# Kernel tuning notes

Measured on AMD Instinct MI355X. Metric: run time of the kernel, lower is better.

The kernel has to match this reference:

```python
import jax, jax.numpy as jnp
import numpy as np

N = 50000
E = 800000
IN_CH = 128
HID = 16
HEADS = 8
OUT_CH = 64
NEG_SLOPE = 0.2


def setup_inputs() -> dict:
    key = jax.random.key(0)
    ks = jax.random.split(key, 16)
    x = jax.random.normal(ks[0], (N, IN_CH), dtype=jnp.float32)
    edge_index = jax.random.randint(ks[1], (2, E), 0, N, dtype=jnp.int64)
    s = 0.05
    # GATv2 layer 1: in=128 -> heads=8, out=16 (concat -> 128)
    W1l = jax.random.normal(ks[2], (IN_CH, HEADS * HID), dtype=jnp.float32) * s
    b1l = jnp.zeros((HEADS * HID,), dtype=jnp.float32)
    W1r = jax.random.normal(ks[3], (IN_CH, HEADS * HID), dtype=jnp.float32) * s
    b1r = jnp.zeros((HEADS * HID,), dtype=jnp.float32)
    att1 = jax.random.normal(ks[4], (HEADS, HID), dtype=jnp.float32) * s
    bias1 = jnp.zeros((HEADS * HID,), dtype=jnp.float32)
    # GATv2 layer 2: in=128 -> heads=1, out=64
    W2l = jax.random.normal(ks[5], (HEADS * HID, OUT_CH), dtype=jnp.float32) * s
    b2l = jnp.zeros((OUT_CH,), dtype=jnp.float32)
    W2r = jax.random.normal(ks[6], (HEADS * HID, OUT_CH), dtype=jnp.float32) * s
    b2r = jnp.zeros((OUT_CH,), dtype=jnp.float32)
    att2 = jax.random.normal(ks[7], (1, OUT_CH), dtype=jnp.float32) * s
    bias2 = jnp.zeros((OUT_CH,), dtype=jnp.float32)
    return dict(x=x, edge_index=edge_index,
                W1l=W1l, b1l=b1l, W1r=W1r, b1r=b1r, att1=att1, bias1=bias1,
                W2l=W2l, b2l=b2l, W2r=W2r, b2r=b2r, att2=att2, bias2=bias2)


def gatv2_conv(x, src, dst, Wl, bl, Wr, br, att, bias, heads, out_ch, concat):
    n = x.shape[0]
    xl = (x @ Wl + bl).reshape(n, heads, out_ch)  # source transform
    xr = (x @ Wr + br).reshape(n, heads, out_ch)  # target transform
    m = xl[src] + xr[dst]                          # [E, H, C]
    m = jnp.where(m > 0, m, NEG_SLOPE * m)         # LeakyReLU(0.2)
    alpha = jnp.einsum('ehc,hc->eh', m, att)       # [E, H]
    # segment softmax over destination nodes (every node has a self loop)
    amax = jax.ops.segment_max(alpha, dst, num_segments=n)
    ea = jnp.exp(alpha - amax[dst])
    denom = jax.ops.segment_sum(ea, dst, num_segments=n)
    w = ea / denom[dst]                            # [E, H]
    out = jax.ops.segment_sum(xl[src] * w[:, :, None], dst, num_segments=n)
    if concat:
        out = out.reshape(n, heads * out_ch)
    else:
        out = out.mean(axis=1)
    return out + bias


def reference(x, edge_index, W1l, b1l, W1r, b1r, att1, bias1,
              W2l, b2l, W2r, b2r, att2, bias2):
    n = x.shape[0]
    loops = jnp.arange(n, dtype=edge_index.dtype)
    src = jnp.concatenate([edge_index[0], loops])
    dst = jnp.concatenate([edge_index[1], loops])
    # dropout layers are identity in eval mode
    h = gatv2_conv(x, src, dst, W1l, b1l, W1r, b1r, att1, bias1,
                   heads=HEADS, out_ch=HID, concat=True)
    h = jax.nn.elu(h)
    out = gatv2_conv(h, src, dst, W2l, b2l, W2r, b2r, att2, bias2,
                     heads=1, out_ch=OUT_CH, concat=True)
    return out
```

## Files before the change

kernel.cpp:

```cpp
#include <hip/hip_runtime.h>
#include <hip/hip_bf16.h>

constexpr int N_  = 50000;
constexpr int E_  = 800000;
constexpr int ET_ = 850000;
constexpr float NEG_SLOPE = 0.2f;

constexpr int SCAN_NB = (N_ + 255) / 256;
constexpr int CSR_CAP = 1250008;
constexpr int HT      = ET_ / 8;
constexpr int HB      = (HT + 255) / 256;
constexpr int G1B     = N_ / 16;
constexpr int ZERO4   = (50000 + CSR_CAP) / 4;

typedef __attribute__((ext_vector_type(8))) short short8;
typedef __attribute__((ext_vector_type(4))) float f32x4;

__device__ inline float leaky(float v) { return fmaxf(v, NEG_SLOPE * v); }

__device__ inline unsigned bf16rn(float f) {
    union { float f; unsigned u; } v; v.f = f;
    return (v.u + 0x7fffu + ((v.u >> 16) & 1u)) >> 16;
}
__device__ inline float2 unpack2(unsigned u) {
    return make_float2(__uint_as_float(u << 16), __uint_as_float(u & 0xffff0000u));
}

__device__ inline int edge_dst(int e, const int* __restrict__ ei) {
    return (e < E_) ? ei[E_ + e] : e - E_;
}
__device__ inline int edge_src(int e, const int* __restrict__ ei) {
    return (e < E_) ? ei[e] : e - E_;
}

__global__ __launch_bounds__(256) void init_kernel(
        const float* __restrict__ W1l, const float* __restrict__ W1r,
        const float* __restrict__ W2l, const float* __restrict__ W2r,
        unsigned short* __restrict__ wsw, unsigned short* __restrict__ wsw2,
        int4* __restrict__ zbase) {
    int gid = blockIdx.x * 256 + threadIdx.x;
    if (gid < ZERO4) zbase[gid] = make_int4(0, 0, 0, 0);
    if (gid < 32768) {
        int j    = gid & 7;
        int lane = (gid >> 3) & 63;
        int ks   = (gid >> 9) & 3;
        int ct   = gid >> 11;
        int k = ks * 32 + ((lane >> 4) & 3) * 8 + j;
        int c = ct * 16 + (lane & 15);
        float v = (c < 128) ? W1l[k * 128 + c] : W1r[k * 128 + (c - 128)];
        wsw[gid] = (unsigned short)bf16rn(v);
    } else if (gid < 49152) {
        int t2   = gid - 32768;
        int j    = t2 & 7;
        int lane = (t2 >> 3) & 63;
        int ks   = (t2 >> 9) & 3;
        int ct   = t2 >> 11;
        int k = ks * 32 + ((lane >> 4) & 3) * 8 + j;
        int c = ct * 16 + (lane & 15);
        float v = (c < 64) ? W2l[k * 64 + c] : W2r[k * 64 + (c - 64)];
        wsw2[t2] = (unsigned short)bf16rn(v);
    }
}

__global__ __launch_bounds__(256) void hist_gemm1(
        const int* __restrict__ ei, int* __restrict__ count, int* __restrict__ off,
        const float* __restrict__ x, const unsigned short* __restrict__ wsw,
        const float* __restrict__ bl, const float* __restrict__ br,
        unsigned short* __restrict__ xlu, float* __restrict__ xr1) {
    if (blockIdx.x < HB) {
        int t = blockIdx.x * 256 + threadIdx.x;
        if (t >= HT) return;
        int e8 = t * 8;
        int d[8], o[8];
        #pragma unroll
        for (int i = 0; i < 8; ++i) d[i] = edge_dst(e8 + i, ei);
        #pragma unroll
        for (int i = 0; i < 8; ++i) o[i] = atomicAdd(&count[d[i]], 1);
        int4* op = (int4*)(off + e8);
        op[0] = make_int4(o[0], o[1], o[2], o[3]);
        op[1] = make_int4(o[4], o[5], o[6], o[7]);
        return;
    }
    const int blk  = blockIdx.x - HB;
    const int wave = threadIdx.x >> 6;
    const int lane = threadIdx.x & 63;
    const int n0 = blk * 16;
    const int m = lane & 15;
    const int q = (lane >> 4) & 3;
    const float* __restrict__ arow = x + (size_t)(n0 + m) * 128 + q * 8;
    short8 afrag[4];
    #pragma unroll
    for (int ks = 0; ks < 4; ++ks) {
        float4 v0 = *(const float4*)(arow + ks * 32);
        float4 v1 = *(const float4*)(arow + ks * 32 + 4);
        short8 a;
        a[0] = (short)bf16rn(v0.x); a[1] = (short)bf16rn(v0.y);
        a[2] = (short)bf16rn(v0.z); a[3] = (short)bf16rn(v0.w);
        a[4] = (short)bf16rn(v1.x); a[5] = (short)bf16rn(v1.y);
        a[6] = (short)bf16rn(v1.z); a[7] = (short)bf16rn(v1.w);
        afrag[ks] = a;
    }
    #pragma unroll
    for (int i = 0; i < 4; ++i) {
        const int ct = wave * 4 + i;
        f32x4 acc = {0.f, 0.f, 0.f, 0.f};
        #pragma unroll
        for (int ks = 0; ks < 4; ++ks) {
            short8 b = *(const short8*)(wsw + ((size_t)(ct * 4 + ks) * 64 + lane) * 8);
            acc = __builtin_amdgcn_mfma_f32_16x16x32_bf16(afrag[ks], b, acc, 0, 0, 0);
        }
        const int col = ct * 16 + m;
        if (ct < 8) {
            float bias = bl[col];
            #pragma unroll
            for (int j = 0; j < 4; ++j) {
                int row = n0 + q * 4 + j;
                xlu[(size_t)row * 128 + col] = (unsigned short)bf16rn(acc[j] + bias);
            }
        } else {
            float bias = br[col - 128];
            #pragma unroll
            for (int j = 0; j < 4; ++j) {
                int row = n0 + q * 4 + j;
                xr1[(size_t)row * 128 + (col - 128)] = acc[j] + bias;
            }
        }
    }
}

__global__ __launch_bounds__(256) void scan_partial(
        const int* __restrict__ count, int* __restrict__ bsum) {
    __shared__ int red[256];
    int t = threadIdx.x;
    int i = blockIdx.x * 256 + t;
    red[t] = (i < N_) ? ((count[i] + 7) & ~7) : 0;
    __syncthreads();
    #pragma unroll
    for (int o = 128; o > 0; o >>= 1) {
        if (t < o) red[t] += red[t + o];
        __syncthreads();
    }
    if (t == 0) bsum[blockIdx.x] = red[0];
}

__global__ __launch_bounds__(256) void scan_final2(
        const int* __restrict__ count, const int* __restrict__ bsum,
        int* __restrict__ start) {
    __shared__ int top[256];
    __shared__ int buf[256];
    int t = threadIdx.x;
    top[t] = (t < SCAN_NB) ? bsum[t] : 0;
    __syncthreads();
    #pragma unroll
    for (int o = 1; o < 256; o <<= 1) {
        int add = (t >= o) ? top[t - o] : 0;
        __syncthreads();
        top[t] += add;
        __syncthreads();
    }
    int bst = (blockIdx.x == 0) ? 0 : top[blockIdx.x - 1];
    int i = blockIdx.x * 256 + t;
    int v = (i < N_) ? ((count[i] + 7) & ~7) : 0;
    buf[t] = v;
    __syncthreads();
    #pragma unroll
    for (int o = 1; o < 256; o <<= 1) {
        int add = (t >= o) ? buf[t - o] : 0;
        __syncthreads();
        buf[t] += add;
        __syncthreads();
    }
    if (i < N_) start[i] = bst + buf[t] - v;
}

__global__ __launch_bounds__(256) void scatter_kernel(
        const int* __restrict__ ei, const int* __restrict__ start,
        const int* __restrict__ off, int* __restrict__ csr_src) {
    int t = blockIdx.x * 256 + threadIdx.x;
    if (t >= HT) return;
    int e8 = t * 8;
    int4 o0 = *(const int4*)(off + e8);
    int4 o1 = *(const int4*)(off + e8 + 4);
    int o[8] = {o0.x, o0.y, o0.z, o0.w, o1.x, o1.y, o1.z, o1.w};
    int s[8], d[8];
    #pragma unroll
    for (int i = 0; i < 8; ++i) {
        s[i] = edge_src(e8 + i, ei);
        d[i] = edge_dst(e8 + i, ei);
    }
    int st[8];
    #pragma unroll
    for (int i = 0; i < 8; ++i) st[i] = start[d[i]];
    #pragma unroll
    for (int i = 0; i < 8; ++i) csr_src[st[i] + o[i]] = s[i];
}

__global__ __launch_bounds__(256) void fused1(
        const int* __restrict__ csr_src, const int* __restrict__ start,
        const int* __restrict__ count,
        const unsigned* __restrict__ xl1b, const float* __restrict__ xr1,
        const float* __restrict__ att, const float* __restrict__ bias1,
        float* __restrict__ hout) {
    int t = blockIdx.x * 256 + threadIdx.x;
    int n = __builtin_amdgcn_readfirstlane(t >> 6);
    int lane = t & 63;
    if (n >= N_) return;
    float2 xr = *(const float2*)(xr1 + (size_t)n * 128 + 2 * lane);
    float2 av = *(const float2*)(att + 2 * lane);
    int p0 = __builtin_amdgcn_readfirstlane(start[n]);
    int p1 = p0 + __builtin_amdgcn_readfirstlane(count[n]);
    float2 acc = make_float2(0.f, 0.f);
    float l = 0.f;
    for (int p = p0; p < p1; p += 4) {
        int4 si = *(const int4*)(csr_src + p);
        int s0 = __builtin_amdgcn_readfirstlane(si.x);
        int s1 = __builtin_amdgcn_readfirstlane(si.y);
        int s2 = __builtin_amdgcn_readfirstlane(si.z);
        int s3 = __builtin_amdgcn_readfirstlane(si.w);
        float2 x0 = unpack2(xl1b[(size_t)s0 * 64 + lane]);
        float2 x1 = unpack2(xl1b[(size_t)s1 * 64 + lane]);
        float2 x2 = unpack2(xl1b[(size_t)s2 * 64 + lane]);
        float2 x3 = unpack2(xl1b[(size_t)s3 * 64 + lane]);
        float a0 = fmaf(leaky(x0.x + xr.x), av.x, leaky(x0.y + xr.y) * av.y);
        float a1 = fmaf(leaky(x1.x + xr.x), av.x, leaky(x1.y + xr.y) * av.y);
        float a2 = fmaf(leaky(x2.x + xr.x), av.x, leaky(x2.y + xr.y) * av.y);
        float a3 = fmaf(leaky(x3.x + xr.x), av.x, leaky(x3.y + xr.y) * av.y);
        a0 += __shfl_xor(a0, 1); a1 += __shfl_xor(a1, 1);
        a2 += __shfl_xor(a2, 1); a3 += __shfl_xor(a3, 1);
        a0 += __shfl_xor(a0, 2); a1 += __shfl_xor(a1, 2);
        a2 += __shfl_xor(a2, 2); a3 += __shfl_xor(a3, 2);
        a0 += __shfl_xor(a0, 4); a1 += __shfl_xor(a1, 4);
        a2 += __shfl_xor(a2, 4); a3 += __shfl_xor(a3, 4);
        float w0 = __expf(a0);
        float w1 = p + 1 < p1 ? __expf(a1) : 0.f;
        float w2 = p + 2 < p1 ? __expf(a2) : 0.f;
        float w3 = p + 3 < p1 ? __expf(a3) : 0.f;
        acc.x = fmaf(w0, x0.x, acc.x); acc.y = fmaf(w0, x0.y, acc.y); l += w0;
        acc.x = fmaf(w1, x1.x, acc.x); acc.y = fmaf(w1, x1.y, acc.y); l += w1;
        acc.x = fmaf(w2, x2.x, acc.x); acc.y = fmaf(w2, x2.y, acc.y); l += w2;
        acc.x = fmaf(w3, x3.x, acc.x); acc.y = fmaf(w3, x3.y, acc.y); l += w3;
    }
    float2 bv = *(const float2*)(bias1 + 2 * lane);
    float vx = acc.x / l + bv.x;
    float vy = acc.y / l + bv.y;
    float2 o;
    o.x = vx > 0.f ? vx : (__expf(vx) - 1.f);
    o.y = vy > 0.f ? vy : (__expf(vy) - 1.f);
    *(float2*)(hout + (size_t)n * 128 + 2 * lane) = o;
}

__global__ __launch_bounds__(256) void gemm2_mfma(
        const float* __restrict__ hbuf,
        const unsigned short* __restrict__ wsw2,
        const float* __restrict__ bl, const float* __restrict__ br,
        unsigned short* __restrict__ xlu2, float* __restrict__ xr2) {
    const int wave = threadIdx.x >> 6;
    const int lane = threadIdx.x & 63;
    const int n0 = blockIdx.x * 16;
    const int m = lane & 15;
    const int q = (lane >> 4) & 3;
    const float* __restrict__ arow = hbuf + (size_t)(n0 + m) * 128 + q * 8;
    short8 afrag[4];
    #pragma unroll
    for (int ks = 0; ks < 4; ++ks) {
        float4 v0 = *(const float4*)(arow + ks * 32);
        float4 v1 = *(const float4*)(arow + ks * 32 + 4);
        short8 a;
        a[0] = (short)bf16rn(v0.x); a[1] = (short)bf16rn(v0.y);
        a[2] = (short)bf16rn(v0.z); a[3] = (short)bf16rn(v0.w);
        a[4] = (short)bf16rn(v1.x); a[5] = (short)bf16rn(v1.y);
        a[6] = (short)bf16rn(v1.z); a[7] = (short)bf16rn(v1.w);
        afrag[ks] = a;
    }
    #pragma unroll
    for (int i = 0; i < 2; ++i) {
        const int ct = wave * 2 + i;
        f32x4 acc = {0.f, 0.f, 0.f, 0.f};
        #pragma unroll
        for (int ks = 0; ks < 4; ++ks) {
            short8 b = *(const short8*)(wsw2 + ((size_t)(ct * 4 + ks) * 64 + lane) * 8);
            acc = __builtin_amdgcn_mfma_f32_16x16x32_bf16(afrag[ks], b, acc, 0, 0, 0);
        }
        const int col = ct * 16 + m;
        if (ct < 4) {
            float bias = bl[col];
            #pragma unroll
            for (int j = 0; j < 4; ++j) {
                int row = n0 + q * 4 + j;
                xlu2[(size_t)row * 64 + col] = (unsigned short)bf16rn(acc[j] + bias);
            }
        } else {
            float bias = br[col - 64];
            #pragma unroll
            for (int j = 0; j < 4; ++j) {
                int row = n0 + q * 4 + j;
                xr2[(size_t)row * 64 + (col - 64)] = acc[j] + bias;
            }
        }
    }
}

__global__ __launch_bounds__(256) void fused2(
        const int* __restrict__ csr_src, const int* __restrict__ start,
        const int* __restrict__ count,
        const unsigned* __restrict__ xl2b, const float* __restrict__ xr2,
        const float* __restrict__ att, const float* __restrict__ bias2,
        float* __restrict__ out) {
    int t = blockIdx.x * 256 + threadIdx.x;
    int n = __builtin_amdgcn_readfirstlane(t >> 6);
    int lane = t & 63;
    int half = lane >> 5;
    int lc   = lane & 31;
    if (n >= N_) return;
    float2 xr = *(const float2*)(xr2 + (size_t)n * 64 + 2 * lc);
    float2 av = *(const float2*)(att + 2 * lc);
    int p0 = __builtin_amdgcn_readfirstlane(start[n]);
    int p1 = p0 + __builtin_amdgcn_readfirstlane(count[n]);
    float2 acc = make_float2(0.f, 0.f);
    float l = 0.f;
    for (int p = p0; p < p1; p += 8) {
        int4 ia = *(const int4*)(csr_src + p);
        int4 ib = *(const int4*)(csr_src + p + 4);
        int sx[8];
        sx[0] = __builtin_amdgcn_readfirstlane(ia.x);
        sx[1] = __builtin_amdgcn_readfirstlane(ia.y);
        sx[2] = __builtin_amdgcn_readfirstlane(ia.z);
        sx[3] = __builtin_amdgcn_readfirstlane(ia.w);
        sx[4] = __builtin_amdgcn_readfirstlane(ib.x);
        sx[5] = __builtin_amdgcn_readfirstlane(ib.y);
        sx[6] = __builtin_amdgcn_readfirstlane(ib.z);
        sx[7] = __builtin_amdgcn_readfirstlane(ib.w);
        #pragma unroll
        for (int u = 0; u < 4; ++u) {
            int pe = p + 2 * u + half;
            int s  = sx[2 * u + half];
            float2 xv = unpack2(xl2b[(size_t)s * 32 + lc]);
            float a = fmaf(leaky(xv.x + xr.x), av.x, leaky(xv.y + xr.y) * av.y);
            a += __shfl_xor(a, 1);
            a += __shfl_xor(a, 2);
            a += __shfl_xor(a, 4);
            a += __shfl_xor(a, 8);
            a += __shfl_xor(a, 16);
            float w = pe < p1 ? __expf(a) : 0.f;
            acc.x = fmaf(w, xv.x, acc.x);
            acc.y = fmaf(w, xv.y, acc.y);
            l += w;
        }
    }
    acc.x += __shfl_xor(acc.x, 32);
    acc.y += __shfl_xor(acc.y, 32);
    l     += __shfl_xor(l, 32);
    if (half == 0) {
        float2 bv = *(const float2*)(bias2 + 2 * lc);
        float2 o;
        o.x = acc.x / l + bv.x;
        o.y = acc.y / l + bv.y;
        *(float2*)(out + (size_t)n * 64 + 2 * lc) = o;
    }
}

extern "C" void kernel_launch(void* const* d_in, const int* in_sizes, int n_in,
                              void* d_out, int out_size, void* d_ws, size_t ws_size,
                              hipStream_t stream) {
    (void)in_sizes; (void)n_in; (void)out_size; (void)ws_size;
    const float* x     = (const float*)d_in[0];
    const int*   ei    = (const int*)d_in[1];
    const float* W1l   = (const float*)d_in[2];
    const float* b1l   = (const float*)d_in[3];
    const float* W1r   = (const float*)d_in[4];
    const float* b1r   = (const float*)d_in[5];
    const float* att1  = (const float*)d_in[6];
    const float* bias1 = (const float*)d_in[7];
    const float* W2l   = (const float*)d_in[8];
    const float* b2l   = (const float*)d_in[9];
    const float* W2r   = (const float*)d_in[10];
    const float* b2r   = (const float*)d_in[11];
    const float* att2  = (const float*)d_in[12];
    const float* bias2 = (const float*)d_in[13];
    float* out = (float*)d_out;

    float* xr1      = (float*)d_ws;
    float* hbuf     = xr1 + 6400000;
    unsigned* xl1b  = (unsigned*)(hbuf + 6400000);
    int* count   = (int*)(xl1b + 3200000);
    int* csr_src = count + 50000;
    int* startp  = csr_src + CSR_CAP;
    int* off     = startp + 50000;
    int* bsum    = off + 850000;
    int* bstart  = bsum + 256;
    unsigned short* wsw2 = (unsigned short*)(bstart + 256);
    unsigned* xl2b = xl1b;
    float* xr2     = xr1;
    unsigned short* wsw = (unsigned short*)hbuf;

    init_kernel<<<(ZERO4 + 255) / 256, 256, 0, stream>>>(W1l, W1r, W2l, W2r,
                                                         wsw, wsw2, (int4*)count);
    hist_gemm1 <<<HB + G1B, 256, 0, stream>>>(ei, count, off, x, wsw, b1l, b1r,
                                              (unsigned short*)xl1b, xr1);
    scan_partial<<<SCAN_NB, 256, 0, stream>>>(count, bsum);
    scan_final2 <<<SCAN_NB, 256, 0, stream>>>(count, bsum, startp);
    scatter_kernel<<<(HT + 255) / 256, 256, 0, stream>>>(ei, startp, off, csr_src);

    fused1<<<(N_ * 64 + 255) / 256, 256, 0, stream>>>(csr_src, startp, count,
                                                      xl1b, xr1, att1, bias1, hbuf);
    gemm2_mfma <<<N_ / 16, 256, 0, stream>>>(hbuf, wsw2, b2l, b2r,
                                             (unsigned short*)xl2b, xr2);
    fused2<<<(N_ * 64 + 255) / 256, 256, 0, stream>>>(csr_src, startp, count,
                                                      xl2b, xr2, att2, bias2, out);
}
```

Baseline: 269.2 us.

## Privatize degree histogram into 8 sub-counters to reduce atomic contention

The destination-degree histogram now uses 8 replicated count arrays, selected by thread index, so atomics on the same node are spread across copies. The partial scan turns the 8 copies into per-copy prefix offsets and writes the total count. The scatter adds the per-copy base to the local offset. This trades extra zero-initialisation, memory and an extra gather for fewer colliding atomics.

```diff
diff --git a/kernel.cpp b/kernel.cpp
--- a/kernel.cpp
+++ b/kernel.cpp
@@ -11,7 +11,7 @@
 constexpr int HT      = ET_ / 8;
 constexpr int HB      = (HT + 255) / 256;
 constexpr int G1B     = N_ / 16;
-constexpr int ZERO4   = (50000 + CSR_CAP) / 4;
+constexpr int ZERO4   = (8 * N_ + CSR_CAP) / 4;
 
 typedef __attribute__((ext_vector_type(8))) short short8;
 typedef __attribute__((ext_vector_type(4))) float f32x4;
@@ -63,19 +63,20 @@
 }
 
 __global__ __launch_bounds__(256) void hist_gemm1(
-        const int* __restrict__ ei, int* __restrict__ count, int* __restrict__ off,
+        const int* __restrict__ ei, int* __restrict__ count8, int* __restrict__ off,
         const float* __restrict__ x, const unsigned short* __restrict__ wsw,
         const float* __restrict__ bl, const float* __restrict__ br,
         unsigned short* __restrict__ xlu, float* __restrict__ xr1) {
     if (blockIdx.x < HB) {
         int t = blockIdx.x * 256 + threadIdx.x;
         if (t >= HT) return;
+        int* __restrict__ cnt = count8 + (t & 7) * N_;
         int e8 = t * 8;
         int d[8], o[8];
         #pragma unroll
         for (int i = 0; i < 8; ++i) d[i] = edge_dst(e8 + i, ei);
         #pragma unroll
-        for (int i = 0; i < 8; ++i) o[i] = atomicAdd(&count[d[i]], 1);
+        for (int i = 0; i < 8; ++i) o[i] = atomicAdd(&cnt[d[i]], 1);
         int4* op = (int4*)(off + e8);
         op[0] = make_int4(o[0], o[1], o[2], o[3]);
         op[1] = make_int4(o[4], o[5], o[6], o[7]);
@@ -129,11 +130,23 @@
 }
 
 __global__ __launch_bounds__(256) void scan_partial(
-        const int* __restrict__ count, int* __restrict__ bsum) {
+        int* __restrict__ count8, int* __restrict__ count, int* __restrict__ bsum) {
     __shared__ int red[256];
     int t = threadIdx.x;
     int i = blockIdx.x * 256 + t;
-    red[t] = (i < N_) ? ((count[i] + 7) & ~7) : 0;
+    int sum = 0;
+    if (i < N_) {
+        int run = 0;
+        #pragma unroll
+        for (int p = 0; p < 8; ++p) {
+            int v = count8[p * N_ + i];
+            count8[p * N_ + i] = run;
+            run += v;
+        }
+        sum = run;
+        count[i] = sum;
+    }
+    red[t] = (i < N_) ? ((sum + 7) & ~7) : 0;
     __syncthreads();
     #pragma unroll
     for (int o = 128; o > 0; o >>= 1) {
@@ -175,9 +188,11 @@
 
 __global__ __launch_bounds__(256) void scatter_kernel(
         const int* __restrict__ ei, const int* __restrict__ start,
-        const int* __restrict__ off, int* __restrict__ csr_src) {
+        const int* __restrict__ off, const int* __restrict__ count8,
+        int* __restrict__ csr_src) {
     int t = blockIdx.x * 256 + threadIdx.x;
     if (t >= HT) return;
+    const int* __restrict__ pp = count8 + (t & 7) * N_;
     int e8 = t * 8;
     int4 o0 = *(const int4*)(off + e8);
     int4 o1 = *(const int4*)(off + e8 + 4);
@@ -188,11 +203,13 @@
         s[i] = edge_src(e8 + i, ei);
         d[i] = edge_dst(e8 + i, ei);
     }
-    int st[8];
+    int st[8], pv[8];
     #pragma unroll
     for (int i = 0; i < 8; ++i) st[i] = start[d[i]];
     #pragma unroll
-    for (int i = 0; i < 8; ++i) csr_src[st[i] + o[i]] = s[i];
+    for (int i = 0; i < 8; ++i) pv[i] = pp[d[i]];
+    #pragma unroll
+    for (int i = 0; i < 8; ++i) csr_src[st[i] + pv[i] + o[i]] = s[i];
 }
 
 __global__ __launch_bounds__(256) void fused1(
@@ -382,24 +399,25 @@
     float* xr1      = (float*)d_ws;
     float* hbuf     = xr1 + 6400000;
     unsigned* xl1b  = (unsigned*)(hbuf + 6400000);
-    int* count   = (int*)(xl1b + 3200000);
-    int* csr_src = count + 50000;
-    int* startp  = csr_src + CSR_CAP;
+    int* count8  = (int*)(xl1b + 3200000);
+    int* csr_src = count8 + 8 * N_;
+    int* count   = csr_src + CSR_CAP;
+    int* startp  = count + 50000;
     int* off     = startp + 50000;
     int* bsum    = off + 850000;
-    int* bstart  = bsum + 256;
-    unsigned short* wsw2 = (unsigned short*)(bstart + 256);
+    unsigned short* wsw2 = (unsigned short*)(bsum + 256);
     unsigned* xl2b = xl1b;
     float* xr2     = xr1;
     unsigned short* wsw = (unsigned short*)hbuf;
 
     init_kernel<<<(ZERO4 + 255) / 256, 256, 0, stream>>>(W1l, W1r, W2l, W2r,
-                                                         wsw, wsw2, (int4*)count);
-    hist_gemm1 <<<HB + G1B, 256, 0, stream>>>(ei, count, off, x, wsw, b1l, b1r,
+                                                         wsw, wsw2, (int4*)count8);
+    hist_gemm1 <<<HB + G1B, 256, 0, stream>>>(ei, count8, off, x, wsw, b1l, b1r,
                                               (unsigned short*)xl1b, xr1);
-    scan_partial<<<SCAN_NB, 256, 0, stream>>>(count, bsum);
+    scan_partial<<<SCAN_NB, 256, 0, stream>>>(count8, count, bsum);
     scan_final2 <<<SCAN_NB, 256, 0, stream>>>(count, bsum, startp);
-    scatter_kernel<<<(HT + 255) / 256, 256, 0, stream>>>(ei, startp, off, csr_src);
+    scatter_kernel<<<(HT + 255) / 256, 256, 0, stream>>>(ei, startp, off,
+                                                         count8, csr_src);
 
     fused1<<<(N_ * 64 + 255) / 256, 256, 0, stream>>>(csr_src, startp, count,
                                                       xl1b, xr1, att1, bias1, hbuf);
```

Result: no change. 272.9 us (+1.4%).
